# Optimization experiments

Hardware: AMD Instinct MI355X
Metric: run time of the kernel (lower is better)

Reference implementation:

```python
import jax, jax.numpy as jnp
import numpy as np

N0, N1, N2 = 200000, 50000, 10000   # node counts per hop (src -> layer1 targets -> layer2 targets)
E1, E2 = 1000000, 250000
C_IN, H = 128, 256


def setup_inputs() -> dict:
    key = jax.random.key(0)
    ks = jax.random.split(key, 10)
    return {
        "x": jax.random.normal(ks[0], (N0, C_IN), dtype=jnp.float32),
        "src1": jax.random.randint(ks[1], (E1,), 0, N0, dtype=jnp.int32),
        "dst1": jax.random.randint(ks[2], (E1,), 0, N1, dtype=jnp.int32),
        "src2": jax.random.randint(ks[3], (E2,), 0, N1, dtype=jnp.int32),
        "dst2": jax.random.randint(ks[4], (E2,), 0, N2, dtype=jnp.int32),
        "Wl1": jax.random.normal(ks[5], (C_IN, H), dtype=jnp.float32) / np.sqrt(C_IN),
        "Wr1": jax.random.normal(ks[6], (C_IN, H), dtype=jnp.float32) / np.sqrt(C_IN),
        "b1": jnp.zeros((H,), dtype=jnp.float32),
        "Wl2": jax.random.normal(ks[7], (H, H), dtype=jnp.float32) / np.sqrt(H),
        "Wr2": jax.random.normal(ks[8], (H, H), dtype=jnp.float32) / np.sqrt(H),
        "b2": jnp.zeros((H,), dtype=jnp.float32),
    }


def _sage_conv(x_src, x_dst, src, dst, Wl, Wr, b, n_dst):
    # mean aggregation of neighbor messages (PyG SAGEConv, aggr='mean', root_weight=True)
    msgs = x_src[src]                                             # [E, C] irregular gather
    agg = jax.ops.segment_sum(msgs, dst, num_segments=n_dst)      # [n_dst, C]
    cnt = jax.ops.segment_sum(jnp.ones_like(dst, dtype=x_src.dtype), dst, num_segments=n_dst)
    agg = agg / jnp.maximum(cnt, 1.0)[:, None]
    return agg @ Wl + x_dst @ Wr + b


def reference(x, src1, dst1, src2, dst2, Wl1, Wr1, b1, Wl2, Wr2, b2):
    # layer 1: targets are first N1 nodes
    h = _sage_conv(x, x[:N1], src1, dst1, Wl1, Wr1, b1, N1)       # [N1, H]
    h = jax.nn.relu(h)                                            # dropout: eval mode (identity)
    # layer 2: targets are first N2 nodes of the layer-1 output
    out = _sage_conv(h, h[:N2], src2, dst2, Wl2, Wr2, b2, N2)     # [N2, H]
    return out
```

## Files before the change

### kernel.cpp

```cpp
#include <hip/hip_runtime.h>

#define N0 200000
#define N1 50000
#define N2 10000
#define E1 1000000
#define E2 250000
#define CIN 128
#define HD  256

#define NB1  196
#define NB2  79
#define CAP1 8192
#define CAP2 4096

#define NBIN1 489
#define NBIN2 123
#define NPREP 768
#define NCVT  25000

typedef __attribute__((ext_vector_type(8))) short short8;
typedef __attribute__((ext_vector_type(4))) float f32x4;

__device__ __forceinline__ unsigned short f2bf(float f) {
    unsigned u = __builtin_bit_cast(unsigned, f);
    u = (u + 0x7fffu + ((u >> 16) & 1u)) >> 16;
    return (unsigned short)u;
}
__device__ __forceinline__ float bf2f(unsigned short h) {
    unsigned u = ((unsigned)h) << 16;
    return __builtin_bit_cast(float, u);
}

template<int SHIFTB, int PACKSH, int CAP>
__device__ __forceinline__ void bin_body(
    int bb, const int* __restrict__ src, const int* __restrict__ dst,
    int* __restrict__ gcnt, unsigned* __restrict__ binned, int E, int* sh)
{
    int* hcnt  = sh;
    int* hbase = sh + 256;
    int* hcur  = sh + 512;
    const int t = threadIdx.x;
    hcnt[t] = 0;
    __syncthreads();

    unsigned pk[8];
    int      bk[8];
    const int e0 = bb * 2048;
    #pragma unroll
    for (int j = 0; j < 8; j++) {
        const int e = e0 + j * 256 + t;
        if (e < E) {
            const int d = dst[e];
            const int s = src[e];
            bk[j] = d >> SHIFTB;
            pk[j] = ((unsigned)(d & ((1 << SHIFTB) - 1)) << PACKSH) | (unsigned)s;
            atomicAdd(&hcnt[bk[j]], 1);
        } else bk[j] = -1;
    }
    __syncthreads();

    hbase[t] = atomicAdd(&gcnt[t], hcnt[t]);
    hcur[t]  = 0;
    __syncthreads();

    #pragma unroll
    for (int j = 0; j < 8; j++) {
        if (bk[j] >= 0) {
            const int idx = atomicAdd(&hcur[bk[j]], 1);
            binned[(size_t)bk[j] * CAP + hbase[bk[j]] + idx] = pk[j];
        }
    }
}

__global__ __launch_bounds__(256) void megaA_kernel(
    const float* __restrict__ x, unsigned short* __restrict__ xb,
    const float* __restrict__ Wl1, const float* __restrict__ Wr1,
    const float* __restrict__ Wl2, const float* __restrict__ Wr2,
    unsigned short* __restrict__ wsw1, unsigned short* __restrict__ wsw2,
    const int* __restrict__ src1, const int* __restrict__ dst1,
    const int* __restrict__ src2, const int* __restrict__ dst2,
    int* __restrict__ gcnt1, int* __restrict__ gcnt2,
    unsigned* __restrict__ binned1, unsigned* __restrict__ binned2)
{
    __shared__ int sh[768];
    const int b = blockIdx.x;
    const int t = threadIdx.x;

    if (b < NBIN1) {
        bin_body<8, 18, CAP1>(b, src1, dst1, gcnt1, binned1, E1, sh);
    } else if (b < NBIN1 + NBIN2) {
        bin_body<7, 16, CAP2>(b - NBIN1, src2, dst2, gcnt2, binned2, E2, sh);
    } else if (b < NBIN1 + NBIN2 + NPREP) {
        const int pb = b - NBIN1 - NBIN2;
        const float* Wl; const float* Wr; unsigned short* wsw; int K, tid;
        if (pb < 256) { Wl = Wl1; Wr = Wr1; wsw = wsw1; K = CIN; tid = pb * 256 + t; }
        else          { Wl = Wl2; Wr = Wr2; wsw = wsw2; K = HD;  tid = (pb - 256) * 256 + t; }
        const int j  = tid & 7;
        const int L  = (tid >> 3) & 63;
        const int nt = (tid >> 9) & 15;
        const int kt = tid >> 13;
        const int k  = kt * 32 + (L >> 4) * 8 + j;
        const int n  = nt * 16 + (L & 15);
        const float v = (k < K) ? Wl[(size_t)k * HD + n]
                                : Wr[(size_t)(k - K) * HD + n];
        wsw[tid] = f2bf(v);
    } else {
        const int i = (b - NBIN1 - NBIN2 - NPREP) * 256 + t;
        const float4 v = ((const float4*)x)[i];
        ushort4 o;
        o.x = f2bf(v.x); o.y = f2bf(v.y); o.z = f2bf(v.z); o.w = f2bf(v.w);
        ((ushort4*)xb)[i] = o;
    }
}

template<int PACKSH, int DPB, int CAP>
__device__ __forceinline__ void bfill_body(
    int b, const unsigned* __restrict__ binned, const int* __restrict__ gcnt,
    int* __restrict__ off, int* __restrict__ deg, int* __restrict__ eid,
    int Ndst, int* lhist, int* lcur, int* ebuf)
{
    const int t = threadIdx.x;
    const int cnt = gcnt[b];
    const unsigned* bp = binned + (size_t)b * CAP;

    if (t < DPB) lhist[t] = 0;
    __syncthreads();

    for (int i = t; i < cnt; i += 256)
        atomicAdd(&lhist[bp[i] >> PACKSH], 1);
    __syncthreads();

    const int h0 = (t < DPB) ? lhist[t] : 0;
    __syncthreads();
    #pragma unroll
    for (int ofs = 1; ofs < DPB; ofs <<= 1) {
        const int u = (t >= ofs && t < DPB) ? lhist[t - ofs] : 0;
        __syncthreads();
        if (t < DPB) lhist[t] += u;
        __syncthreads();
    }

    if (t < DPB) {
        const int excl = lhist[t] - h0;
        lcur[t] = excl;
        const int d = b * DPB + t;
        if (d < Ndst) {
            off[d] = b * CAP + excl;
            deg[d] = h0;
        }
    }
    __syncthreads();

    for (int i = t; i < cnt; i += 256) {
        const unsigned p = bp[i];
        const int slot = atomicAdd(&lcur[p >> PACKSH], 1);
        ebuf[slot] = (int)(p & ((1u << PACKSH) - 1u));
    }
    __syncthreads();

    for (int i = t; i < cnt; i += 256)
        eid[(size_t)b * CAP + i] = ebuf[i];
}

__global__ __launch_bounds__(256) void bfill_both(
    const unsigned* __restrict__ binned1, const int* __restrict__ gcnt1,
    int* __restrict__ off1, int* __restrict__ deg1, int* __restrict__ eid1,
    const unsigned* __restrict__ binned2, const int* __restrict__ gcnt2,
    int* __restrict__ off2, int* __restrict__ deg2, int* __restrict__ eid2)
{
    __shared__ int lhist[256], lcur[256];
    __shared__ int ebuf[CAP1];
    if (blockIdx.x < NB1)
        bfill_body<18, 256, CAP1>(blockIdx.x, binned1, gcnt1,
                                  off1, deg1, eid1, N1, lhist, lcur, ebuf);
    else
        bfill_body<16, 128, CAP2>(blockIdx.x - NB1, binned2, gcnt2,
                                  off2, deg2, eid2, N2, lhist, lcur, ebuf);
}

__global__ __launch_bounds__(256) void gather_k128b(
    const unsigned short* __restrict__ xb, const int* __restrict__ eid,
    const int* __restrict__ off, const int* __restrict__ deg,
    unsigned short* __restrict__ agg)
{
    const int w = blockIdx.x * 4 + (threadIdx.x >> 6);
    const int lane = threadIdx.x & 63;
    const int half = lane >> 5;
    const int l32  = lane & 31;
    const int base = off[w];
    const int n    = deg[w];

    float ax = 0.f, ay = 0.f, az = 0.f, aw = 0.f;
    int i = half;
    for (; i + 6 < n; i += 8) {
        const int s0 = eid[base + i];
        const int s1 = eid[base + i + 2];
        const int s2 = eid[base + i + 4];
        const int s3 = eid[base + i + 6];
        const ushort4 v0 = *(const ushort4*)(xb + (size_t)s0 * CIN + l32 * 4);
        const ushort4 v1 = *(const ushort4*)(xb + (size_t)s1 * CIN + l32 * 4);
        const ushort4 v2 = *(const ushort4*)(xb + (size_t)s2 * CIN + l32 * 4);
        const ushort4 v3 = *(const ushort4*)(xb + (size_t)s3 * CIN + l32 * 4);
        ax += bf2f(v0.x) + bf2f(v1.x) + bf2f(v2.x) + bf2f(v3.x);
        ay += bf2f(v0.y) + bf2f(v1.y) + bf2f(v2.y) + bf2f(v3.y);
        az += bf2f(v0.z) + bf2f(v1.z) + bf2f(v2.z) + bf2f(v3.z);
        aw += bf2f(v0.w) + bf2f(v1.w) + bf2f(v2.w) + bf2f(v3.w);
    }
    for (; i < n; i += 2) {
        const int s = eid[base + i];
        const ushort4 v = *(const ushort4*)(xb + (size_t)s * CIN + l32 * 4);
        ax += bf2f(v.x); ay += bf2f(v.y); az += bf2f(v.z); aw += bf2f(v.w);
    }
    ax += __shfl_xor(ax, 32);
    ay += __shfl_xor(ay, 32);
    az += __shfl_xor(az, 32);
    aw += __shfl_xor(aw, 32);

    if (half == 0) {
        const float s = 1.0f / fmaxf((float)n, 1.0f);
        ushort4 o;
        o.x = f2bf(ax * s); o.y = f2bf(ay * s);
        o.z = f2bf(az * s); o.w = f2bf(aw * s);
        *(ushort4*)(agg + (size_t)w * CIN + l32 * 4) = o;
    }
}

__global__ __launch_bounds__(256) void gather_k256b(
    const unsigned short* __restrict__ hb, const int* __restrict__ eid,
    const int* __restrict__ off, const int* __restrict__ deg,
    unsigned short* __restrict__ agg)
{
    const int w = blockIdx.x * 4 + (threadIdx.x >> 6);
    const int lane = threadIdx.x & 63;
    const int base = off[w];
    const int n    = deg[w];

    float ax = 0.f, ay = 0.f, az = 0.f, aw = 0.f;
    int i = 0;
    for (; i + 3 < n; i += 4) {
        const int s0 = eid[base + i];
        const int s1 = eid[base + i + 1];
        const int s2 = eid[base + i + 2];
        const int s3 = eid[base + i + 3];
        const ushort4 v0 = *(const ushort4*)(hb + (size_t)s0 * HD + lane * 4);
        const ushort4 v1 = *(const ushort4*)(hb + (size_t)s1 * HD + lane * 4);
        const ushort4 v2 = *(const ushort4*)(hb + (size_t)s2 * HD + lane * 4);
        const ushort4 v3 = *(const ushort4*)(hb + (size_t)s3 * HD + lane * 4);
        ax += bf2f(v0.x) + bf2f(v1.x) + bf2f(v2.x) + bf2f(v3.x);
        ay += bf2f(v0.y) + bf2f(v1.y) + bf2f(v2.y) + bf2f(v3.y);
        az += bf2f(v0.z) + bf2f(v1.z) + bf2f(v2.z) + bf2f(v3.z);
        aw += bf2f(v0.w) + bf2f(v1.w) + bf2f(v2.w) + bf2f(v3.w);
    }
    for (; i < n; i++) {
        const int s = eid[base + i];
        const ushort4 v = *(const ushort4*)(hb + (size_t)s * HD + lane * 4);
        ax += bf2f(v.x); ay += bf2f(v.y); az += bf2f(v.z); aw += bf2f(v.w);
    }
    const float s = 1.0f / fmaxf((float)n, 1.0f);
    ushort4 o;
    o.x = f2bf(ax * s); o.y = f2bf(ay * s);
    o.z = f2bf(az * s); o.w = f2bf(aw * s);
    *(ushort4*)(agg + (size_t)w * HD + lane * 4) = o;
}

template<int K1, int K2, bool RELU, bool OUTBF>
__global__ __launch_bounds__(256) void mfma_gemm(
    const unsigned short* __restrict__ A1, const unsigned short* __restrict__ A2,
    const unsigned short* __restrict__ wsw, const float* __restrict__ bias,
    void* __restrict__ outp, int M)
{
    constexpr int KT1 = K1 / 32;
    constexpr int KT  = (K1 + K2) / 32;

    const int t = threadIdx.x;
    const int w = t >> 6;
    const int L = t & 63;
    const int m = L & 15;
    const int q = L >> 4;
    const int row0 = blockIdx.x * 64;

    const unsigned short* a1p[4];
    const unsigned short* a2p[4];
    #pragma unroll
    for (int rg = 0; rg < 4; rg++) {
        const int r = min(row0 + rg * 16 + m, M - 1);
        a1p[rg] = A1 + (size_t)r * K1 + q * 8;
        a2p[rg] = A2 + (size_t)r * K2 + q * 8;
    }

    f32x4 acc[4][4];
    #pragma unroll
    for (int rg = 0; rg < 4; rg++)
        #pragma unroll
        for (int tt = 0; tt < 4; tt++)
            acc[rg][tt] = (f32x4){0.f, 0.f, 0.f, 0.f};

    #pragma unroll
    for (int kt = 0; kt < KT; kt++) {
        short8 bfr[4];
        #pragma unroll
        for (int tt = 0; tt < 4; tt++)
            bfr[tt] = *(const short8*)(
                wsw + (((size_t)kt * 16 + (w * 4 + tt)) * 64 + L) * 8);
        #pragma unroll
        for (int rg = 0; rg < 4; rg++) {
            short8 af;
            if (kt < KT1) af = *(const short8*)(a1p[rg] + kt * 32);
            else          af = *(const short8*)(a2p[rg] + (kt - KT1) * 32);
            #pragma unroll
            for (int tt = 0; tt < 4; tt++)
                acc[rg][tt] = __builtin_amdgcn_mfma_f32_16x16x32_bf16(
                    af, bfr[tt], acc[rg][tt], 0, 0, 0);
        }
    }

    #pragma unroll
    for (int rg = 0; rg < 4; rg++) {
        const int orow0 = row0 + rg * 16 + q * 4;
        #pragma unroll
        for (int tt = 0; tt < 4; tt++) {
            const int col = (w * 4 + tt) * 16 + m;
            const float bv = bias[col];
            #pragma unroll
            for (int r = 0; r < 4; r++) {
                const int row = orow0 + r;
                if (row < M) {
                    float v = acc[rg][tt][r] + bv;
                    if (RELU) v = fmaxf(v, 0.0f);
                    const size_t idx = (size_t)row * HD + col;
                    if (OUTBF) ((unsigned short*)outp)[idx] = f2bf(v);
                    else       ((float*)outp)[idx] = v;
                }
            }
        }
    }
}

extern "C" void kernel_launch(void* const* d_in, const int* in_sizes, int n_in,
                              void* d_out, int out_size, void* d_ws, size_t ws_size,
                              hipStream_t stream)
{
    const float* x    = (const float*)d_in[0];
    const int*   src1 = (const int*)  d_in[1];
    const int*   dst1 = (const int*)  d_in[2];
    const int*   src2 = (const int*)  d_in[3];
    const int*   dst2 = (const int*)  d_in[4];
    const float* Wl1  = (const float*)d_in[5];
    const float* Wr1  = (const float*)d_in[6];
    const float* b1   = (const float*)d_in[7];
    const float* Wl2  = (const float*)d_in[8];
    const float* Wr2  = (const float*)d_in[9];
    const float* b2   = (const float*)d_in[10];
    float* out = (float*)d_out;

    unsigned short* xb   = (unsigned short*)d_ws;
    unsigned short* hb   = xb + (size_t)N1 * CIN;
    unsigned short* agg1 = xb + (size_t)N0 * CIN;
    unsigned short* agg2 = agg1 + (size_t)N1 * CIN;
    unsigned short* wsw1 = agg2 + (size_t)N2 * HD;
    unsigned short* wsw2 = wsw1 + 2 * CIN * HD;
    int* gcnt1 = (int*)(wsw2 + 2 * HD * HD);
    int* gcnt2 = gcnt1 + 256;
    int* off1  = gcnt2 + 256;
    int* deg1  = off1 + N1;
    int* off2  = deg1 + N1;
    int* deg2  = off2 + N2;
    unsigned* binned1 = (unsigned*)(deg2 + N2);
    int*      eid1    = (int*)(binned1 + (size_t)NB1 * CAP1);
    unsigned* binned2 = (unsigned*)(eid1 + (size_t)NB1 * CAP1);
    int*      eid2    = (int*)(binned2 + (size_t)NB2 * CAP2);

    hipMemsetAsync(gcnt1, 0, 512 * sizeof(int), stream);

    megaA_kernel<<<NBIN1 + NBIN2 + NPREP + NCVT, 256, 0, stream>>>(
        x, xb, Wl1, Wr1, Wl2, Wr2, wsw1, wsw2,
        src1, dst1, src2, dst2, gcnt1, gcnt2, binned1, binned2);

    bfill_both<<<NB1 + NB2, 256, 0, stream>>>(
        binned1, gcnt1, off1, deg1, eid1,
        binned2, gcnt2, off2, deg2, eid2);

    gather_k128b<<<N1 / 4, 256, 0, stream>>>(xb, eid1, off1, deg1, agg1);
    mfma_gemm<CIN, CIN, true, true><<<(N1 + 63) / 64, 256, 0, stream>>>(
        agg1, xb, wsw1, b1, hb, N1);

    gather_k256b<<<N2 / 4, 256, 0, stream>>>(hb, eid2, off2, deg2, agg2);
    mfma_gemm<HD, HD, false, false><<<(N2 + 63) / 64, 256, 0, stream>>>(
        agg2, hb, wsw2, b2, out, N2);
}
```

Measured before the change: 314.1 us.

## Fuse CSR fill, neighbor gather and GEMM into one kernel per layer

Replaces the separate bucket-fill, gather and MFMA GEMM kernels with one fused kernel per layer. Each block sorts its bin's edges in shared memory, aggregates neighbor means into an MFMA-ready shared tile, then multiplies by the concatenated weights. Bins are halved (128/64 destinations) to fit shared memory. This removes launches and the global eid/off/deg/agg round trips, at the cost of fewer, larger blocks with heavy LDS use and a GEMM that reads weights per block.

```diff
diff --git a/kernel.cpp b/kernel.cpp
--- a/kernel.cpp
+++ b/kernel.cpp
@@ -8,10 +8,16 @@
 #define CIN 128
 #define HD  256
 
-#define NB1  196
-#define NB2  79
-#define CAP1 8192
-#define CAP2 4096
+#define SH1   7
+#define PK1   18
+#define NB1   391
+#define CAP1  3072
+#define DPB1  128
+#define SH2   6
+#define PK2   16
+#define NB2   157
+#define CAP2  2048
+#define DPB2  64
 
 #define NBIN1 489
 #define NBIN2 123
@@ -37,10 +43,10 @@
     int* __restrict__ gcnt, unsigned* __restrict__ binned, int E, int* sh)
 {
     int* hcnt  = sh;
-    int* hbase = sh + 256;
-    int* hcur  = sh + 512;
+    int* hbase = sh + 512;
+    int* hcur  = sh + 1024;
     const int t = threadIdx.x;
-    hcnt[t] = 0;
+    hcnt[t] = 0; hcnt[t + 256] = 0;
     __syncthreads();
 
     unsigned pk[8];
@@ -59,8 +65,8 @@
     }
     __syncthreads();
 
-    hbase[t] = atomicAdd(&gcnt[t], hcnt[t]);
-    hcur[t]  = 0;
+    hbase[t]       = atomicAdd(&gcnt[t], hcnt[t]);             hcur[t] = 0;
+    hbase[t + 256] = atomicAdd(&gcnt[t + 256], hcnt[t + 256]); hcur[t + 256] = 0;
     __syncthreads();
 
     #pragma unroll
@@ -82,14 +88,14 @@
     int* __restrict__ gcnt1, int* __restrict__ gcnt2,
     unsigned* __restrict__ binned1, unsigned* __restrict__ binned2)
 {
-    __shared__ int sh[768];
+    __shared__ int sh[1536];
     const int b = blockIdx.x;
     const int t = threadIdx.x;
 
     if (b < NBIN1) {
-        bin_body<8, 18, CAP1>(b, src1, dst1, gcnt1, binned1, E1, sh);
+        bin_body<SH1, PK1, CAP1>(b, src1, dst1, gcnt1, binned1, E1, sh);
     } else if (b < NBIN1 + NBIN2) {
-        bin_body<7, 16, CAP2>(b - NBIN1, src2, dst2, gcnt2, binned2, E2, sh);
+        bin_body<SH2, PK2, CAP2>(b - NBIN1, src2, dst2, gcnt2, binned2, E2, sh);
     } else if (b < NBIN1 + NBIN2 + NPREP) {
         const int pb = b - NBIN1 - NBIN2;
         const float* Wl; const float* Wr; unsigned short* wsw; int K, tid;
@@ -113,225 +119,233 @@
     }
 }
 
-template<int PACKSH, int DPB, int CAP>
-__device__ __forceinline__ void bfill_body(
-    int b, const unsigned* __restrict__ binned, const int* __restrict__ gcnt,
-    int* __restrict__ off, int* __restrict__ deg, int* __restrict__ eid,
-    int Ndst, int* lhist, int* lcur, int* ebuf)
-{
+__global__ __launch_bounds__(512) void layer1_mega(
+    const unsigned short* __restrict__ xb,
+    const unsigned* __restrict__ binned1, const int* __restrict__ gcnt1,
+    const unsigned short* __restrict__ wsw1, const float* __restrict__ bias,
+    unsigned short* __restrict__ hb)
+{
+    __shared__ int ebuf[CAP1];
+    __shared__ int lhist[DPB1], loff[DPB1], lcur[DPB1];
+    __shared__ __align__(16) unsigned short aggT[4 * 128 * 4 * 8];
+
     const int t = threadIdx.x;
-    const int cnt = gcnt[b];
-    const unsigned* bp = binned + (size_t)b * CAP;
-
-    if (t < DPB) lhist[t] = 0;
-    __syncthreads();
-
-    for (int i = t; i < cnt; i += 256)
-        atomicAdd(&lhist[bp[i] >> PACKSH], 1);
-    __syncthreads();
-
-    const int h0 = (t < DPB) ? lhist[t] : 0;
-    __syncthreads();
-    #pragma unroll
-    for (int ofs = 1; ofs < DPB; ofs <<= 1) {
-        const int u = (t >= ofs && t < DPB) ? lhist[t - ofs] : 0;
+    const int b = blockIdx.x;
+    const int cnt = gcnt1[b];
+    const unsigned* bp = binned1 + (size_t)b * CAP1;
+
+    if (t < DPB1) lhist[t] = 0;
+    __syncthreads();
+    for (int i = t; i < cnt; i += 512)
+        atomicAdd(&lhist[bp[i] >> PK1], 1);
+    __syncthreads();
+    const int h0 = (t < DPB1) ? lhist[t] : 0;
+    __syncthreads();
+    #pragma unroll
+    for (int ofs = 1; ofs < DPB1; ofs <<= 1) {
+        const int u = (t >= ofs && t < DPB1) ? lhist[t - ofs] : 0;
         __syncthreads();
-        if (t < DPB) lhist[t] += u;
+        if (t < DPB1) lhist[t] += u;
         __syncthreads();
     }
-
-    if (t < DPB) {
-        const int excl = lhist[t] - h0;
-        lcur[t] = excl;
-        const int d = b * DPB + t;
-        if (d < Ndst) {
-            off[d] = b * CAP + excl;
-            deg[d] = h0;
-        }
-    }
-    __syncthreads();
-
-    for (int i = t; i < cnt; i += 256) {
+    if (t < DPB1) { loff[t] = lhist[t] - h0; lcur[t] = lhist[t] - h0; }
+    __syncthreads();
+    for (int i = t; i < cnt; i += 512) {
         const unsigned p = bp[i];
-        const int slot = atomicAdd(&lcur[p >> PACKSH], 1);
-        ebuf[slot] = (int)(p & ((1u << PACKSH) - 1u));
-    }
-    __syncthreads();
-
-    for (int i = t; i < cnt; i += 256)
-        eid[(size_t)b * CAP + i] = ebuf[i];
-}
-
-__global__ __launch_bounds__(256) void bfill_both(
-    const unsigned* __restrict__ binned1, const int* __restrict__ gcnt1,
-    int* __restrict__ off1, int* __restrict__ deg1, int* __restrict__ eid1,
+        const int slot = atomicAdd(&lcur[p >> PK1], 1);
+        ebuf[slot] = (int)(p & ((1u << PK1) - 1u));
+    }
+    __syncthreads();
+
+    const int w = t >> 6, L = t & 63, half = L >> 5, l32 = L & 31;
+    const int ktw = l32 >> 3, qw = (l32 >> 1) & 3, jo = (l32 & 1) * 4;
+    for (int r = w; r < DPB1; r += 8) {
+        const int rg = b * DPB1 + r;
+        if (rg < N1) {
+            const int base = loff[r];
+            const int n    = lcur[r] - loff[r];
+            float ax = 0.f, ay = 0.f, az = 0.f, aw = 0.f;
+            int i = half;
+            for (; i + 6 < n; i += 8) {
+                const int s0 = ebuf[base + i];
+                const int s1 = ebuf[base + i + 2];
+                const int s2 = ebuf[base + i + 4];
+                const int s3 = ebuf[base + i + 6];
+                const ushort4 v0 = *(const ushort4*)(xb + (size_t)s0 * CIN + l32 * 4);
+                const ushort4 v1 = *(const ushort4*)(xb + (size_t)s1 * CIN + l32 * 4);
+                const ushort4 v2 = *(const ushort4*)(xb + (size_t)s2 * CIN + l32 * 4);
+                const ushort4 v3 = *(const ushort4*)(xb + (size_t)s3 * CIN + l32 * 4);
+                ax += bf2f(v0.x) + bf2f(v1.x) + bf2f(v2.x) + bf2f(v3.x);
+                ay += bf2f(v0.y) + bf2f(v1.y) + bf2f(v2.y) + bf2f(v3.y);
+                az += bf2f(v0.z) + bf2f(v1.z) + bf2f(v2.z) + bf2f(v3.z);
+                aw += bf2f(v0.w) + bf2f(v1.w) + bf2f(v2.w) + bf2f(v3.w);
+            }
+            for (; i < n; i += 2) {
+                const int s = ebuf[base + i];
+                const ushort4 v = *(const ushort4*)(xb + (size_t)s * CIN + l32 * 4);
+                ax += bf2f(v.x); ay += bf2f(v.y); az += bf2f(v.z); aw += bf2f(v.w);
+            }
+            ax += __shfl_xor(ax, 32);
+            ay += __shfl_xor(ay, 32);
+            az += __shfl_xor(az, 32);
+            aw += __shfl_xor(aw, 32);
+            if (half == 0) {
+                const float s = 1.0f / fmaxf((float)n, 1.0f);
+                ushort4 o;
+                o.x = f2bf(ax * s); o.y = f2bf(ay * s);
+                o.z = f2bf(az * s); o.w = f2bf(aw * s);
+                *(ushort4*)&aggT[(((ktw * 128 + r) * 4 + qw) * 8) + jo] = o;
+            }
+        }
+    }
+    __syncthreads();
+
+    const int m = L & 15, q = L >> 4;
+    const int row_l = w * 16 + m;
+    const int rg2 = min(b * DPB1 + row_l, N1 - 1);
+    const unsigned short* a2p = xb + (size_t)rg2 * CIN + q * 8;
+
+    f32x4 acc[16];
+    #pragma unroll
+    for (int nt = 0; nt < 16; nt++) acc[nt] = (f32x4){0.f, 0.f, 0.f, 0.f};
+
+    #pragma unroll
+    for (int kt = 0; kt < 8; kt++) {
+        short8 af;
+        if (kt < 4) af = *(const short8*)&aggT[((kt * 128 + row_l) * 4 + q) * 8];
+        else        af = *(const short8*)(a2p + (kt - 4) * 32);
+        #pragma unroll
+        for (int nt = 0; nt < 16; nt++) {
+            const short8 bf = *(const short8*)(
+                wsw1 + (((size_t)kt * 16 + nt) * 64 + L) * 8);
+            acc[nt] = __builtin_amdgcn_mfma_f32_16x16x32_bf16(af, bf, acc[nt], 0, 0, 0);
+        }
+    }
+
+    const int orow0 = b * DPB1 + w * 16 + q * 4;
+    #pragma unroll
+    for (int nt = 0; nt < 16; nt++) {
+        const int col = nt * 16 + m;
+        const float bv = bias[col];
+        #pragma unroll
+        for (int r = 0; r < 4; r++) {
+            const int row = orow0 + r;
+            if (row < N1) {
+                const float v = fmaxf(acc[nt][r] + bv, 0.0f);
+                hb[(size_t)row * HD + col] = f2bf(v);
+            }
+        }
+    }
+}
+
+__global__ __launch_bounds__(512) void layer2_mega(
+    const unsigned short* __restrict__ hb,
     const unsigned* __restrict__ binned2, const int* __restrict__ gcnt2,
-    int* __restrict__ off2, int* __restrict__ deg2, int* __restrict__ eid2)
-{
-    __shared__ int lhist[256], lcur[256];
-    __shared__ int ebuf[CAP1];
-    if (blockIdx.x < NB1)
-        bfill_body<18, 256, CAP1>(blockIdx.x, binned1, gcnt1,
-                                  off1, deg1, eid1, N1, lhist, lcur, ebuf);
-    else
-        bfill_body<16, 128, CAP2>(blockIdx.x - NB1, binned2, gcnt2,
-                                  off2, deg2, eid2, N2, lhist, lcur, ebuf);
-}
-
-__global__ __launch_bounds__(256) void gather_k128b(
-    const unsigned short* __restrict__ xb, const int* __restrict__ eid,
-    const int* __restrict__ off, const int* __restrict__ deg,
-    unsigned short* __restrict__ agg)
-{
-    const int w = blockIdx.x * 4 + (threadIdx.x >> 6);
-    const int lane = threadIdx.x & 63;
-    const int half = lane >> 5;
-    const int l32  = lane & 31;
-    const int base = off[w];
-    const int n    = deg[w];
-
-    float ax = 0.f, ay = 0.f, az = 0.f, aw = 0.f;
-    int i = half;
-    for (; i + 6 < n; i += 8) {
-        const int s0 = eid[base + i];
-        const int s1 = eid[base + i + 2];
-        const int s2 = eid[base + i + 4];
-        const int s3 = eid[base + i + 6];
-        const ushort4 v0 = *(const ushort4*)(xb + (size_t)s0 * CIN + l32 * 4);
-        const ushort4 v1 = *(const ushort4*)(xb + (size_t)s1 * CIN + l32 * 4);
-        const ushort4 v2 = *(const ushort4*)(xb + (size_t)s2 * CIN + l32 * 4);
-        const ushort4 v3 = *(const ushort4*)(xb + (size_t)s3 * CIN + l32 * 4);
-        ax += bf2f(v0.x) + bf2f(v1.x) + bf2f(v2.x) + bf2f(v3.x);
-        ay += bf2f(v0.y) + bf2f(v1.y) + bf2f(v2.y) + bf2f(v3.y);
-        az += bf2f(v0.z) + bf2f(v1.z) + bf2f(v2.z) + bf2f(v3.z);
-        aw += bf2f(v0.w) + bf2f(v1.w) + bf2f(v2.w) + bf2f(v3.w);
-    }
-    for (; i < n; i += 2) {
-        const int s = eid[base + i];
-        const ushort4 v = *(const ushort4*)(xb + (size_t)s * CIN + l32 * 4);
-        ax += bf2f(v.x); ay += bf2f(v.y); az += bf2f(v.z); aw += bf2f(v.w);
-    }
-    ax += __shfl_xor(ax, 32);
-    ay += __shfl_xor(ay, 32);
-    az += __shfl_xor(az, 32);
-    aw += __shfl_xor(aw, 32);
-
-    if (half == 0) {
-        const float s = 1.0f / fmaxf((float)n, 1.0f);
-        ushort4 o;
-        o.x = f2bf(ax * s); o.y = f2bf(ay * s);
-        o.z = f2bf(az * s); o.w = f2bf(aw * s);
-        *(ushort4*)(agg + (size_t)w * CIN + l32 * 4) = o;
-    }
-}
-
-__global__ __launch_bounds__(256) void gather_k256b(
-    const unsigned short* __restrict__ hb, const int* __restrict__ eid,
-    const int* __restrict__ off, const int* __restrict__ deg,
-    unsigned short* __restrict__ agg)
-{
-    const int w = blockIdx.x * 4 + (threadIdx.x >> 6);
-    const int lane = threadIdx.x & 63;
-    const int base = off[w];
-    const int n    = deg[w];
-
-    float ax = 0.f, ay = 0.f, az = 0.f, aw = 0.f;
-    int i = 0;
-    for (; i + 3 < n; i += 4) {
-        const int s0 = eid[base + i];
-        const int s1 = eid[base + i + 1];
-        const int s2 = eid[base + i + 2];
-        const int s3 = eid[base + i + 3];
-        const ushort4 v0 = *(const ushort4*)(hb + (size_t)s0 * HD + lane * 4);
-        const ushort4 v1 = *(const ushort4*)(hb + (size_t)s1 * HD + lane * 4);
-        const ushort4 v2 = *(const ushort4*)(hb + (size_t)s2 * HD + lane * 4);
-        const ushort4 v3 = *(const ushort4*)(hb + (size_t)s3 * HD + lane * 4);
-        ax += bf2f(v0.x) + bf2f(v1.x) + bf2f(v2.x) + bf2f(v3.x);
-        ay += bf2f(v0.y) + bf2f(v1.y) + bf2f(v2.y) + bf2f(v3.y);
-        az += bf2f(v0.z) + bf2f(v1.z) + bf2f(v2.z) + bf2f(v3.z);
-        aw += bf2f(v0.w) + bf2f(v1.w) + bf2f(v2.w) + bf2f(v3.w);
-    }
-    for (; i < n; i++) {
-        const int s = eid[base + i];
-        const ushort4 v = *(const ushort4*)(hb + (size_t)s * HD + lane * 4);
-        ax += bf2f(v.x); ay += bf2f(v.y); az += bf2f(v.z); aw += bf2f(v.w);
-    }
-    const float s = 1.0f / fmaxf((float)n, 1.0f);
-    ushort4 o;
-    o.x = f2bf(ax * s); o.y = f2bf(ay * s);
-    o.z = f2bf(az * s); o.w = f2bf(aw * s);
-    *(ushort4*)(agg + (size_t)w * HD + lane * 4) = o;
-}
-
-template<int K1, int K2, bool RELU, bool OUTBF>
-__global__ __launch_bounds__(256) void mfma_gemm(
-    const unsigned short* __restrict__ A1, const unsigned short* __restrict__ A2,
-    const unsigned short* __restrict__ wsw, const float* __restrict__ bias,
-    void* __restrict__ outp, int M)
-{
-    constexpr int KT1 = K1 / 32;
-    constexpr int KT  = (K1 + K2) / 32;
+    const unsigned short* __restrict__ wsw2, const float* __restrict__ bias,
+    float* __restrict__ outp)
+{
+    __shared__ int ebuf[CAP2];
+    __shared__ int lhist[DPB2], loff[DPB2], lcur[DPB2];
+    __shared__ __align__(16) unsigned short aggT[8 * 64 * 4 * 8];
 
     const int t = threadIdx.x;
-    const int w = t >> 6;
-    const int L = t & 63;
-    const int m = L & 15;
-    const int q = L >> 4;
-    const int row0 = blockIdx.x * 64;
-
-    const unsigned short* a1p[4];
-    const unsigned short* a2p[4];
-    #pragma unroll
-    for (int rg = 0; rg < 4; rg++) {
-        const int r = min(row0 + rg * 16 + m, M - 1);
-        a1p[rg] = A1 + (size_t)r * K1 + q * 8;
-        a2p[rg] = A2 + (size_t)r * K2 + q * 8;
-    }
-
-    f32x4 acc[4][4];
-    #pragma unroll
-    for (int rg = 0; rg < 4; rg++)
+    const int b = blockIdx.x;
+    const int cnt = gcnt2[b];
+    const unsigned* bp = binned2 + (size_t)b * CAP2;
+
+    if (t < DPB2) lhist[t] = 0;
+    __syncthreads();
+    for (int i = t; i < cnt; i += 512)
+        atomicAdd(&lhist[bp[i] >> PK2], 1);
+    __syncthreads();
+    const int h0 = (t < DPB2) ? lhist[t] : 0;
+    __syncthreads();
+    #pragma unroll
+    for (int ofs = 1; ofs < DPB2; ofs <<= 1) {
+        const int u = (t >= ofs && t < DPB2) ? lhist[t - ofs] : 0;
+        __syncthreads();
+        if (t < DPB2) lhist[t] += u;
+        __syncthreads();
+    }
+    if (t < DPB2) { loff[t] = lhist[t] - h0; lcur[t] = lhist[t] - h0; }
+    __syncthreads();
+    for (int i = t; i < cnt; i += 512) {
+        const unsigned p = bp[i];
+        const int slot = atomicAdd(&lcur[p >> PK2], 1);
+        ebuf[slot] = (int)(p & ((1u << PK2) - 1u));
+    }
+    __syncthreads();
+
+    const int w = t >> 6, L = t & 63;
+    const int kt2 = L >> 3, q2 = (L >> 1) & 3, jo2 = (L & 1) * 4;
+    for (int r = w; r < DPB2; r += 8) {
+        const int rg = b * DPB2 + r;
+        if (rg < N2) {
+            const int base = loff[r];
+            const int n    = lcur[r] - loff[r];
+            float ax = 0.f, ay = 0.f, az = 0.f, aw = 0.f;
+            int i = 0;
+            for (; i + 3 < n; i += 4) {
+                const int s0 = ebuf[base + i];
+                const int s1 = ebuf[base + i + 1];
+                const int s2 = ebuf[base + i + 2];
+                const int s3 = ebuf[base + i + 3];
+                const ushort4 v0 = *(const ushort4*)(hb + (size_t)s0 * HD + L * 4);
+                const ushort4 v1 = *(const ushort4*)(hb + (size_t)s1 * HD + L * 4);
+                const ushort4 v2 = *(const ushort4*)(hb + (size_t)s2 * HD + L * 4);
+                const ushort4 v3 = *(const ushort4*)(hb + (size_t)s3 * HD + L * 4);
+                ax += bf2f(v0.x) + bf2f(v1.x) + bf2f(v2.x) + bf2f(v3.x);
+                ay += bf2f(v0.y) + bf2f(v1.y) + bf2f(v2.y) + bf2f(v3.y);
+                az += bf2f(v0.z) + bf2f(v1.z) + bf2f(v2.z) + bf2f(v3.z);
+                aw += bf2f(v0.w) + bf2f(v1.w) + bf2f(v2.w) + bf2f(v3.w);
+            }
+            for (; i < n; i++) {
+                const int s = ebuf[base + i];
+                const ushort4 v = *(const ushort4*)(hb + (size_t)s * HD + L * 4);
+                ax += bf2f(v.x); ay += bf2f(v.y); az += bf2f(v.z); aw += bf2f(v.w);
+            }
+            const float s = 1.0f / fmaxf((float)n, 1.0f);
+            ushort4 o;
+            o.x = f2bf(ax * s); o.y = f2bf(ay * s);
+            o.z = f2bf(az * s); o.w = f2bf(aw * s);
+            *(ushort4*)&aggT[(((kt2 * 64 + r) * 4 + q2) * 8) + jo2] = o;
+        }
+    }
+    __syncthreads();
+
+    const int m = L & 15, q = L >> 4;
+    const int mt = w & 3, nh = w >> 2;
+    const int row_l = mt * 16 + m;
+    const int rg2 = min(b * DPB2 + row_l, N2 - 1);
+    const unsigned short* a2p = hb + (size_t)rg2 * HD + q * 8;
+
+    f32x4 acc[8];
+    #pragma unroll
+    for (int nt = 0; nt < 8; nt++) acc[nt] = (f32x4){0.f, 0.f, 0.f, 0.f};
+
+    #pragma unroll
+    for (int kt = 0; kt < 16; kt++) {
+        short8 af;
+        if (kt < 8) af = *(const short8*)&aggT[((kt * 64 + row_l) * 4 + q) * 8];
+        else        af = *(const short8*)(a2p + (kt - 8) * 32);
         #pragma unroll
-        for (int tt = 0; tt < 4; tt++)
-            acc[rg][tt] = (f32x4){0.f, 0.f, 0.f, 0.f};
-
-    #pragma unroll
-    for (int kt = 0; kt < KT; kt++) {
-        short8 bfr[4];
+        for (int nt = 0; nt < 8; nt++) {
+            const short8 bf = *(const short8*)(
+                wsw2 + (((size_t)kt * 16 + (nh * 8 + nt)) * 64 + L) * 8);
+            acc[nt] = __builtin_amdgcn_mfma_f32_16x16x32_bf16(af, bf, acc[nt], 0, 0, 0);
+        }
+    }
+
+    const int orow0 = b * DPB2 + mt * 16 + q * 4;
+    #pragma unroll
+    for (int nt = 0; nt < 8; nt++) {
+        const int col = (nh * 8 + nt) * 16 + m;
+        const float bv = bias[col];
         #pragma unroll
-        for (int tt = 0; tt < 4; tt++)
-            bfr[tt] = *(const short8*)(
-                wsw + (((size_t)kt * 16 + (w * 4 + tt)) * 64 + L) * 8);
-        #pragma unroll
-        for (int rg = 0; rg < 4; rg++) {
-            short8 af;
-            if (kt < KT1) af = *(const short8*)(a1p[rg] + kt * 32);
-            else          af = *(const short8*)(a2p[rg] + (kt - KT1) * 32);
-            #pragma unroll
-            for (int tt = 0; tt < 4; tt++)
-                acc[rg][tt] = __builtin_amdgcn_mfma_f32_16x16x32_bf16(
-                    af, bfr[tt], acc[rg][tt], 0, 0, 0);
-        }
-    }
-
-    #pragma unroll
-    for (int rg = 0; rg < 4; rg++) {
-        const int orow0 = row0 + rg * 16 + q * 4;
-        #pragma unroll
-        for (int tt = 0; tt < 4; tt++) {
-            const int col = (w * 4 + tt) * 16 + m;
-            const float bv = bias[col];
-            #pragma unroll
-            for (int r = 0; r < 4; r++) {
-                const int row = orow0 + r;
-                if (row < M) {
-                    float v = acc[rg][tt][r] + bv;
-                    if (RELU) v = fmaxf(v, 0.0f);
-                    const size_t idx = (size_t)row * HD + col;
-                    if (OUTBF) ((unsigned short*)outp)[idx] = f2bf(v);
-                    else       ((float*)outp)[idx] = v;
-                }
-            }
+        for (int r = 0; r < 4; r++) {
+            const int row = orow0 + r;
+            if (row < N2)
+                outp[(size_t)row * HD + col] = acc[nt][r] + bv;
         }
     }
 }
@@ -354,37 +368,20 @@
     float* out = (float*)d_out;
 
     unsigned short* xb   = (unsigned short*)d_ws;
-    unsigned short* hb   = xb + (size_t)N1 * CIN;
-    unsigned short* agg1 = xb + (size_t)N0 * CIN;
-    unsigned short* agg2 = agg1 + (size_t)N1 * CIN;
-    unsigned short* wsw1 = agg2 + (size_t)N2 * HD;
+    unsigned short* hb   = xb + (size_t)N0 * CIN;
+    unsigned short* wsw1 = hb + (size_t)N1 * HD;
     unsigned short* wsw2 = wsw1 + 2 * CIN * HD;
     int* gcnt1 = (int*)(wsw2 + 2 * HD * HD);
-    int* gcnt2 = gcnt1 + 256;
-    int* off1  = gcnt2 + 256;
-    int* deg1  = off1 + N1;
-    int* off2  = deg1 + N1;
-    int* deg2  = off2 + N2;
-    unsigned* binned1 = (unsigned*)(deg2 + N2);
-    int*      eid1    = (int*)(binned1 + (size_t)NB1 * CAP1);
-    unsigned* binned2 = (unsigned*)(eid1 + (size_t)NB1 * CAP1);
-    int*      eid2    = (int*)(binned2 + (size_t)NB2 * CAP2);
-
-    hipMemsetAsync(gcnt1, 0, 512 * sizeof(int), stream);
+    int* gcnt2 = gcnt1 + 512;
+    unsigned* binned1 = (unsigned*)(gcnt2 + 512);
+    unsigned* binned2 = binned1 + (size_t)NB1 * CAP1;
+
+    hipMemsetAsync(gcnt1, 0, 1024 * sizeof(int), stream);
 
     megaA_kernel<<<NBIN1 + NBIN2 + NPREP + NCVT, 256, 0, stream>>>(
         x, xb, Wl1, Wr1, Wl2, Wr2, wsw1, wsw2,
         src1, dst1, src2, dst2, gcnt1, gcnt2, binned1, binned2);
 
-    bfill_both<<<NB1 + NB2, 256, 0, stream>>>(
-        binned1, gcnt1, off1, deg1, eid1,
-        binned2, gcnt2, off2, deg2, eid2);
-
-    gather_k128b<<<N1 / 4, 256, 0, stream>>>(xb, eid1, off1, deg1, agg1);
-    mfma_gemm<CIN, CIN, true, true><<<(N1 + 63) / 64, 256, 0, stream>>>(
-        agg1, xb, wsw1, b1, hb, N1);
-
-    gather_k256b<<<N2 / 4, 256, 0, stream>>>(hb, eid2, off2, deg2, agg2);
-    mfma_gemm<HD, HD, false, false><<<(N2 + 63) / 64, 256, 0, stream>>>(
-        agg2, hb, wsw2, b2, out, N2);
-}
+    layer1_mega<<<NB1, 512, 0, stream>>>(xb, binned1, gcnt1, wsw1, b1, hb);
+    layer2_mega<<<NB2, 512, 0, stream>>>(hb, binned2, gcnt2, wsw2, b2, out);
+}
```

After: 310.2 us. Within noise of the previous version (-1.2%).
